# Performance work log

Measured on AMD Instinct MI355X. Metric: run time of the kernel, lower is better.

## Reference

```python
import jax, jax.numpy as jnp
import numpy as np

M, K, N = 8192, 4096, 4096

def setup_inputs() -> dict:
    key = jax.random.key(0)
    k1, k2, k3, k4, k5, k6 = jax.random.split(key, 6)
    # quantized activations (per-token symmetric int8)
    x_q = jax.random.randint(k1, (M, K), -128, 128, dtype=jnp.int32).astype(jnp.int8)
    # quantized weight (asymmetric per-output-channel): w_fp16 = scale_weight * (w_q + zp_weight)
    weight = jax.random.randint(k2, (N, K), -128, 128, dtype=jnp.int32).astype(jnp.int8)
    scale_input = (jax.random.uniform(k3, (M,), jnp.float32) * 0.009 + 0.001).astype(jnp.float16)
    scale_weight = (jax.random.uniform(k4, (N,), jnp.float32) * 0.009 + 0.001).astype(jnp.float16)
    zp_weight = jax.random.randint(k5, (N,), 100, 156, dtype=jnp.int32).astype(jnp.int16)
    bias = (jax.random.normal(k6, (N,), jnp.float32) * 0.01).astype(jnp.float16)
    # per-row sum of quantized activations (needed for zero-point correction)
    sum_input = jnp.sum(x_q.astype(jnp.int32), axis=-1).astype(jnp.float32)
    return {
        "input": x_q,
        "weight": weight,
        "bias": bias,
        "scale_input": scale_input,
        "scale_weight": scale_weight,
        "sum_input": sum_input,
        "zp_weight": zp_weight,
    }

def reference(input, weight, bias, scale_input, scale_weight, sum_input, zp_weight):
    acc = jnp.matmul(input.astype(jnp.int32), weight.astype(jnp.int32).T)
    # asymmetric weight zero-point correction: + zp_n * sum_k(x_q[m, k])
    corr = sum_input[:, None] * zp_weight.astype(jnp.float32)[None, :]
    # fused dequant epilogue: per-row activation scale * per-col weight scale, + bias
    scale = scale_input.astype(jnp.float32)[:, None] * scale_weight.astype(jnp.float32)[None, :]
    out = (acc.astype(jnp.float32) + corr) * scale + bias.astype(jnp.float32)[None, :]
    return out.astype(jnp.float16)
```

## Files before the change

### kernel.cpp

```cpp
#include <hip/hip_runtime.h>
#include <stdint.h>


#define BM 256
#define BN 256
#define BK 128

typedef __attribute__((ext_vector_type(4))) int int32x4;
typedef __attribute__((ext_vector_type(16))) int int32x16;

__device__ __forceinline__ void async_copy16(const uint8_t* g, uint8_t* l) {
  __builtin_amdgcn_global_load_lds(
      (const __attribute__((address_space(1))) uint32_t*)(const void*)g,
      (__attribute__((address_space(3))) uint32_t*)l,
      16, 0, 0);
}

__global__ __launch_bounds__(256) void pack_kernel(
    const int* __restrict__ A, const int* __restrict__ B,
    uint8_t* __restrict__ A8, uint8_t* __restrict__ B8,
    int nA4, int nTot4) {
  const int stride = gridDim.x * blockDim.x;
  for (int t = blockIdx.x * blockDim.x + threadIdx.x; t < nTot4; t += stride) {
    const int32x4* src;
    uint32_t* dst;
    if (t < nA4) {
      src = (const int32x4*)A + t;
      dst = (uint32_t*)A8 + t;
    } else {
      int u = t - nA4;
      src = (const int32x4*)B + u;
      dst = (uint32_t*)B8 + u;
    }
    int32x4 v = __builtin_nontemporal_load(src);
    *dst = (uint32_t)(v.x & 255) | ((uint32_t)(v.y & 255) << 8) |
           ((uint32_t)(v.z & 255) << 16) | ((uint32_t)(v.w & 255) << 24);
  }
}

__device__ __forceinline__ void stage_tile(
    const uint8_t* Ab, const uint8_t* Bb, size_t sK, int k0,
    uint8_t* AsBuf, uint8_t* BsBuf, int ldst) {
#pragma unroll
  for (int p = 0; p < 4; ++p)
    async_copy16(Ab + (size_t)(p * 64) * sK + k0, AsBuf + p * 8192 + ldst);
#pragma unroll
  for (int p = 0; p < 4; ++p)
    async_copy16(Bb + (size_t)(p * 64) * sK + k0, BsBuf + p * 8192 + ldst);
}

__global__ __launch_bounds__(512, 2) void w8a8_gemm(
    const uint8_t* __restrict__ A8, const uint8_t* __restrict__ B8,
    const float* __restrict__ bias,
    const float* __restrict__ s_in,
    const float* __restrict__ s_w,
    const float* __restrict__ sum_in,
    const int* __restrict__ zp_w,
    float* __restrict__ out,
    int M, int N, int K) {
  __shared__ uint8_t As[2][BM * BK];
  __shared__ uint8_t Bs[2][BN * BK];

  const int tid = threadIdx.x;
  const int nbn = N / BN;
  int wgs = blockIdx.x;
  if ((gridDim.x & 7) == 0) {
    const int q = gridDim.x >> 3;
    wgs = (blockIdx.x & 7) * q + (blockIdx.x >> 3);
  }
  const int bm = wgs / nbn, bn = wgs % nbn;
  const int row0 = bm * BM, col0 = bn * BN;

  const int wave = tid >> 6, lane = tid & 63;
  const int m32 = lane & 31, half = lane >> 5;
  const int wm = (wave >> 2) * 128;
  const int wn = (wave & 3) * 64;
  const size_t sK = (size_t)K;

  const int row_s = tid >> 3;
  const int cg = (tid & 7) ^ ((tid >> 4) & 7);
  const int ldst = tid * 16;

  const uint8_t* Ab = A8 + (size_t)(row0 + row_s) * sK + cg * 16;
  const uint8_t* Bb = B8 + (size_t)(col0 + row_s) * sK + cg * 16;

  int32x16 acc[4][2] = {};

  const int NT = K / BK;
  stage_tile(Ab, Bb, sK, 0, &As[0][0], &Bs[0][0], ldst);
  if (NT > 1) stage_tile(Ab, Bb, sK, BK, &As[1][0], &Bs[1][0], ldst);

  int cur = 0;
  const int swzr = (m32 >> 1) & 7;
  for (int kt = 0; kt < NT; ++kt) {
    if (kt + 1 < NT) {
      asm volatile("s_waitcnt vmcnt(8)" ::: "memory");
    } else {
      asm volatile("s_waitcnt vmcnt(0)" ::: "memory");
    }
    __builtin_amdgcn_s_barrier();

    const uint8_t* Ac = &As[cur][0];
    const uint8_t* Bc = &Bs[cur][0];
    __builtin_amdgcn_s_setprio(1);
#pragma unroll
    for (int ks = 0; ks < 4; ++ks) {
      const int gran = ((ks * 2 + half) ^ swzr) * 16;
      int32x4 afrag[4], bfrag[2];
#pragma unroll
      for (int i = 0; i < 4; ++i)
        afrag[i] = *(const int32x4*)&Ac[(wm + i * 32 + m32) * BK + gran];
#pragma unroll
      for (int j = 0; j < 2; ++j)
        bfrag[j] = *(const int32x4*)&Bc[(wn + j * 32 + m32) * BK + gran];
#pragma unroll
      for (int i = 0; i < 4; ++i)
#pragma unroll
        for (int j = 0; j < 2; ++j)
          acc[i][j] = __builtin_amdgcn_mfma_i32_32x32x32_i8(
              afrag[i], bfrag[j], acc[i][j], 0, 0, 0);
    }
    __builtin_amdgcn_s_setprio(0);
    asm volatile("s_waitcnt lgkmcnt(0)" ::: "memory");
    __builtin_amdgcn_s_barrier();
    if (kt + 2 < NT)
      stage_tile(Ab, Bb, sK, (kt + 2) * BK, &As[cur][0], &Bs[cur][0], ldst);
    cur ^= 1;
  }

  float swj[2], zpj[2], bj[2];
#pragma unroll
  for (int j = 0; j < 2; ++j) {
    int gc = col0 + wn + j * 32 + m32;
    swj[j] = s_w[gc];
    zpj[j] = (float)zp_w[gc];
    bj[j] = bias[gc];
  }
#pragma unroll
  for (int i = 0; i < 4; ++i) {
#pragma unroll
    for (int reg = 0; reg < 16; ++reg) {
      int gr = row0 + wm + i * 32 + (reg & 3) + 8 * (reg >> 2) + 4 * half;
      float siv = s_in[gr];
      float suv = sum_in[gr];
      float* orow = out + (size_t)gr * N + col0 + wn + m32;
#pragma unroll
      for (int j = 0; j < 2; ++j) {
        float v = ((float)acc[i][j][reg] + suv * zpj[j]) * (siv * swj[j]) + bj[j];
        __builtin_nontemporal_store(v, &orow[j * 32]);
      }
    }
  }
}

__global__ __launch_bounds__(256) void w8a8_gemm_fallback(
    const int* __restrict__ A32, const int* __restrict__ B32,
    const float* __restrict__ bias,
    const float* __restrict__ s_in,
    const float* __restrict__ s_w,
    const float* __restrict__ sum_in,
    const int* __restrict__ zp_w,
    float* __restrict__ out,
    int M, int N, int K) {
  __shared__ uint8_t As[128 * 64];
  __shared__ uint8_t Bs[128 * 64];
  const int tid = threadIdx.x;
  const int bm = blockIdx.y, bn = blockIdx.x;
  const int row0 = bm * 128, col0 = bn * 128;
  const int wave = tid >> 6, lane = tid & 63;
  const int quad = lane >> 4, r = lane & 15;
  const int wm = (wave >> 1) * 64, wn = (wave & 1) * 64;
  const int lin = tid * 16;
  const int srow = lin >> 6;
  const int scol = lin & 63;
  const size_t sK = (size_t)K;
  int32x4 acc[4][4] = {};
  for (int k0 = 0; k0 < K; k0 += 64) {
#pragma unroll
    for (int c = 0; c < 2; ++c) {
      const int* ag = A32 + (size_t)(row0 + srow + c * 64) * sK + k0 + scol;
      const int* bg = B32 + (size_t)(col0 + srow + c * 64) * sK + k0 + scol;
      int32x4 pa, pb;
#pragma unroll
      for (int q = 0; q < 4; ++q) {
        int4 va = ((const int4*)ag)[q];
        int4 vb = ((const int4*)bg)[q];
        pa[q] = (int)((uint32_t)(va.x & 255) | ((uint32_t)(va.y & 255) << 8) |
                      ((uint32_t)(va.z & 255) << 16) | ((uint32_t)(va.w & 255) << 24));
        pb[q] = (int)((uint32_t)(vb.x & 255) | ((uint32_t)(vb.y & 255) << 8) |
                      ((uint32_t)(vb.z & 255) << 16) | ((uint32_t)(vb.w & 255) << 24));
      }
      *(int32x4*)&As[lin + c * 4096] = pa;
      *(int32x4*)&Bs[lin + c * 4096] = pb;
    }
    __syncthreads();
    int32x4 afrag[4], bfrag[4];
#pragma unroll
    for (int i = 0; i < 4; ++i)
      afrag[i] = *(const int32x4*)&As[(wm + i * 16 + r) * 64 + quad * 16];
#pragma unroll
    for (int j = 0; j < 4; ++j)
      bfrag[j] = *(const int32x4*)&Bs[(wn + j * 16 + r) * 64 + quad * 16];
#pragma unroll
    for (int i = 0; i < 4; ++i)
#pragma unroll
      for (int j = 0; j < 4; ++j)
        acc[i][j] = __builtin_amdgcn_mfma_i32_16x16x64_i8(afrag[i], bfrag[j],
                                                          acc[i][j], 0, 0, 0);
    __syncthreads();
  }
  float swj[4], zpj[4], bj[4];
#pragma unroll
  for (int j = 0; j < 4; ++j) {
    int gc = col0 + wn + j * 16 + r;
    swj[j] = s_w[gc];
    zpj[j] = (float)zp_w[gc];
    bj[j] = bias[gc];
  }
#pragma unroll
  for (int i = 0; i < 4; ++i) {
#pragma unroll
    for (int t = 0; t < 4; ++t) {
      int gr = row0 + wm + i * 16 + quad * 4 + t;
      float siv = s_in[gr];
      float suv = sum_in[gr];
      float* orow = out + (size_t)gr * N + col0 + wn + r;
#pragma unroll
      for (int j = 0; j < 4; ++j) {
        float v = ((float)acc[i][j][t] + suv * zpj[j]) * (siv * swj[j]) + bj[j];
        orow[j * 16] = v;
      }
    }
  }
}

extern "C" void kernel_launch(void* const* d_in, const int* in_sizes, int n_in,
                              void* d_out, int out_size, void* d_ws, size_t ws_size,
                              hipStream_t stream) {
  const int* x_q = (const int*)d_in[0];
  const int* w_q = (const int*)d_in[1];
  const float* bias = (const float*)d_in[2];
  const float* s_in = (const float*)d_in[3];
  const float* s_w = (const float*)d_in[4];
  const float* sum_in = (const float*)d_in[5];
  const int* zp_w = (const int*)d_in[6];
  float* out = (float*)d_out;

  const int M = in_sizes[3];
  const int N = in_sizes[2];
  const int K = in_sizes[0] / M;

  const size_t needA = (size_t)M * K;
  const size_t needB = (size_t)N * K;

  if (ws_size >= needA + needB && (M % BM) == 0 && (N % BN) == 0 &&
      (K % BK) == 0) {
    uint8_t* A8 = (uint8_t*)d_ws;
    uint8_t* B8 = A8 + needA;
    const int nA4 = (int)(needA / 4);
    const int nTot4 = (int)((needA + needB) / 4);
    int nblk = (nTot4 + 255) / 256;
    if (nblk > 2048) nblk = 2048;
    pack_kernel<<<nblk, 256, 0, stream>>>(x_q, w_q, A8, B8, nA4, nTot4);
    dim3 grid((M / BM) * (N / BN)), block(512);
    w8a8_gemm<<<grid, block, 0, stream>>>(A8, B8, bias, s_in, s_w, sum_in,
                                          zp_w, out, M, N, K);
  } else {
    dim3 grid(N / 128, M / 128), block(256);
    w8a8_gemm_fallback<<<grid, block, 0, stream>>>(x_q, w_q, bias, s_in, s_w,
                                                   sum_in, zp_w, out, M, N, K);
  }
}
```

Before: 405.6 us.

## Interleave next-tile async loads with MFMA substeps and drop XCD block remap

The old pipeline prefetched two tiles ahead and ended each K iteration with a barrier plus a bulk refill. It now prefetches one tile ahead, issuing two of the eight async global-to-LDS copies inside each of the four k-substeps. Barriers are added per substep, and the loop waits for vmcnt(0) at the start of every iteration. The XCD-aware block remapping is removed in favour of a plain 2D grid. This spreads load issue across the compute phase, but it shortens prefetch depth, adds barriers, and may hurt L2 locality across XCDs.

```diff
diff --git a/kernel.cpp b/kernel.cpp
--- a/kernel.cpp
+++ b/kernel.cpp
@@ -38,17 +38,6 @@
   }
 }
 
-__device__ __forceinline__ void stage_tile(
-    const uint8_t* Ab, const uint8_t* Bb, size_t sK, int k0,
-    uint8_t* AsBuf, uint8_t* BsBuf, int ldst) {
-#pragma unroll
-  for (int p = 0; p < 4; ++p)
-    async_copy16(Ab + (size_t)(p * 64) * sK + k0, AsBuf + p * 8192 + ldst);
-#pragma unroll
-  for (int p = 0; p < 4; ++p)
-    async_copy16(Bb + (size_t)(p * 64) * sK + k0, BsBuf + p * 8192 + ldst);
-}
-
 __global__ __launch_bounds__(512, 2) void w8a8_gemm(
     const uint8_t* __restrict__ A8, const uint8_t* __restrict__ B8,
     const float* __restrict__ bias,
@@ -62,13 +51,7 @@
   __shared__ uint8_t Bs[2][BN * BK];
 
   const int tid = threadIdx.x;
-  const int nbn = N / BN;
-  int wgs = blockIdx.x;
-  if ((gridDim.x & 7) == 0) {
-    const int q = gridDim.x >> 3;
-    wgs = (blockIdx.x & 7) * q + (blockIdx.x >> 3);
-  }
-  const int bm = wgs / nbn, bn = wgs % nbn;
+  const int bm = blockIdx.y, bn = blockIdx.x;
   const int row0 = bm * BM, col0 = bn * BN;
 
   const int wave = tid >> 6, lane = tid & 63;
@@ -87,22 +70,26 @@
   int32x16 acc[4][2] = {};
 
   const int NT = K / BK;
-  stage_tile(Ab, Bb, sK, 0, &As[0][0], &Bs[0][0], ldst);
-  if (NT > 1) stage_tile(Ab, Bb, sK, BK, &As[1][0], &Bs[1][0], ldst);
+#pragma unroll
+  for (int p = 0; p < 4; ++p)
+    async_copy16(Ab + (size_t)(p * 64) * sK, &As[0][p * 8192 + ldst]);
+#pragma unroll
+  for (int p = 0; p < 4; ++p)
+    async_copy16(Bb + (size_t)(p * 64) * sK, &Bs[0][p * 8192 + ldst]);
 
   int cur = 0;
   const int swzr = (m32 >> 1) & 7;
   for (int kt = 0; kt < NT; ++kt) {
-    if (kt + 1 < NT) {
-      asm volatile("s_waitcnt vmcnt(8)" ::: "memory");
-    } else {
-      asm volatile("s_waitcnt vmcnt(0)" ::: "memory");
-    }
+    asm volatile("s_waitcnt vmcnt(0)" ::: "memory");
     __builtin_amdgcn_s_barrier();
 
     const uint8_t* Ac = &As[cur][0];
     const uint8_t* Bc = &Bs[cur][0];
-    __builtin_amdgcn_s_setprio(1);
+    uint8_t* Anx = &As[cur ^ 1][0];
+    uint8_t* Bnx = &Bs[cur ^ 1][0];
+    const int knx = (kt + 1) * BK;
+    const bool more = (kt + 1 < NT);
+
 #pragma unroll
     for (int ks = 0; ks < 4; ++ks) {
       const int gran = ((ks * 2 + half) ^ swzr) * 16;
@@ -113,18 +100,35 @@
 #pragma unroll
       for (int j = 0; j < 2; ++j)
         bfrag[j] = *(const int32x4*)&Bc[(wn + j * 32 + m32) * BK + gran];
+      if (more) {
+        if (ks < 2) {
+#pragma unroll
+          for (int p = 0; p < 2; ++p) {
+            const int pa = ks * 2 + p;
+            async_copy16(Ab + (size_t)(pa * 64) * sK + knx,
+                         Anx + pa * 8192 + ldst);
+          }
+        } else {
+#pragma unroll
+          for (int p = 0; p < 2; ++p) {
+            const int pb = (ks - 2) * 2 + p;
+            async_copy16(Bb + (size_t)(pb * 64) * sK + knx,
+                         Bnx + pb * 8192 + ldst);
+          }
+        }
+      }
+      __builtin_amdgcn_s_barrier();
+      asm volatile("s_waitcnt lgkmcnt(0)" ::: "memory");
+      __builtin_amdgcn_s_setprio(1);
 #pragma unroll
       for (int i = 0; i < 4; ++i)
 #pragma unroll
         for (int j = 0; j < 2; ++j)
           acc[i][j] = __builtin_amdgcn_mfma_i32_32x32x32_i8(
               afrag[i], bfrag[j], acc[i][j], 0, 0, 0);
-    }
-    __builtin_amdgcn_s_setprio(0);
-    asm volatile("s_waitcnt lgkmcnt(0)" ::: "memory");
-    __builtin_amdgcn_s_barrier();
-    if (kt + 2 < NT)
-      stage_tile(Ab, Bb, sK, (kt + 2) * BK, &As[cur][0], &Bs[cur][0], ldst);
+      __builtin_amdgcn_s_setprio(0);
+      if (ks < 3) __builtin_amdgcn_s_barrier();
+    }
     cur ^= 1;
   }
 
@@ -254,7 +258,7 @@
   const size_t needB = (size_t)N * K;
 
   if (ws_size >= needA + needB && (M % BM) == 0 && (N % BN) == 0 &&
-      (K % BK) == 0) {
+      (K % BK) == 0 && (K / BK) >= 2) {
     uint8_t* A8 = (uint8_t*)d_ws;
     uint8_t* B8 = A8 + needA;
     const int nA4 = (int)(needA / 4);
@@ -262,7 +266,7 @@
     int nblk = (nTot4 + 255) / 256;
     if (nblk > 2048) nblk = 2048;
     pack_kernel<<<nblk, 256, 0, stream>>>(x_q, w_q, A8, B8, nA4, nTot4);
-    dim3 grid((M / BM) * (N / BN)), block(512);
+    dim3 grid(N / BN, M / BM), block(512);
     w8a8_gemm<<<grid, block, 0, stream>>>(A8, B8, bias, s_in, s_w, sum_in,
                                           zp_w, out, M, N, K);
   } else {
```

Result: faster. 392.5 us (-3.2%).
